# Performance work log

Measured on AMD Instinct MI355X. Metric: run time of the kernel, lower is better.

The kernel has to match this reference:

```python
import jax, jax.numpy as jnp
import numpy as np

# (in_dim, out_dim) for fc1..fc14, hard-coded in the torch module
DIMS = [(12,12),(12,11),(11,10),(10,9),(9,8),(8,7),(7,6),(6,7),(7,8),(8,9),(9,10),(10,11),(11,12),(12,2)]
BATCH = 2_000_000


def setup_inputs() -> dict:
    key = jax.random.key(0)
    keys = jax.random.split(key, 2 * len(DIMS) + 1)
    inp = {"x": jax.random.normal(keys[0], (BATCH, 12), dtype=jnp.float32)}
    for i, (din, dout) in enumerate(DIMS):
        s = 1.0 / np.sqrt(din)  # torch nn.Linear default init range
        inp[f"w{i+1}"] = jax.random.uniform(keys[2*i+1], (dout, din), jnp.float32, -s, s)
        inp[f"b{i+1}"] = jax.random.uniform(keys[2*i+2], (dout,), jnp.float32, -s, s)
    return inp


def _forward(x, Ws, Bs):
    lin = lambda h, i: h @ Ws[i].T + Bs[i]
    # encoder half: fc1..fc6 with ReLU, saving identities 1..6
    ids = []
    h = x
    for i in range(6):
        h = jax.nn.relu(lin(h, i))
        ids.append(h)
    # bottleneck fc7
    h = jax.nn.relu(lin(h, 6))
    # decoder half: fc8..fc13, each adds the matching identity before ReLU
    # fc8 (+id6), fc9 (+id5), ..., fc13 (+id1)
    for i in range(7, 13):
        h = jax.nn.relu(lin(h, i) + ids[12 - i])
    # fc14 + softmax over class dim
    return jax.nn.softmax(lin(h, 13), axis=1)


def reference(x, w1, b1, w2, b2, w3, b3, w4, b4, w5, b5, w6, b6, w7, b7,
              w8, b8, w9, b9, w10, b10, w11, b11, w12, b12, w13, b13, w14, b14):
    Ws = [w1, w2, w3, w4, w5, w6, w7, w8, w9, w10, w11, w12, w13, w14]
    Bs = [b1, b2, b3, b4, b5, b6, b7, b8, b9, b10, b11, b12, b13, b14]
    return _forward(x, Ws, Bs)
```

## Files before the change

kernel.cpp:

```cpp
#include <hip/hip_runtime.h>
#include <math.h>

#define DEV __device__ __forceinline__

typedef float f2 __attribute__((ext_vector_type(2)));

DEV f2 splat(float s) { f2 r; r.x = s; r.y = s; return r; }


#define OW1  0
#define OB1  144
#define OW2  156
#define OB2  288
#define OW3  300
#define OB3  412
#define OW4  424
#define OB4  516
#define OW5  528
#define OB5  600
#define OW6  608
#define OB6  664
#define OW7  672
#define OB7  716
#define OW8  724
#define OB8  768
#define OW9  776
#define OB9  832
#define OW10 840
#define OB10 912
#define OW11 924
#define OB11 1016
#define OW12 1028
#define OB12 1140
#define OW13 1152
#define OB13 1284
#define OW14 1296
#define OB14 1320
#define WTOT 1324

__device__ __attribute__((aligned(16))) float Wpack[WTOT];

__global__ void repack_kernel(
    const float* w1,  const float* b1,  const float* w2,  const float* b2,
    const float* w3,  const float* b3,  const float* w4,  const float* b4,
    const float* w5,  const float* b5,  const float* w6,  const float* b6,
    const float* w7,  const float* b7,  const float* w8,  const float* b8,
    const float* w9,  const float* b9,  const float* w10, const float* b10,
    const float* w11, const float* b11, const float* w12, const float* b12,
    const float* w13, const float* b13, const float* w14, const float* b14) {
    struct Seg { const float* src; int dst; int len; };
    const Seg segs[28] = {
        {w1,  OW1,  144}, {b1,  OB1,  12}, {w2,  OW2,  132}, {b2,  OB2,  11},
        {w3,  OW3,  110}, {b3,  OB3,  10}, {w4,  OW4,   90}, {b4,  OB4,   9},
        {w5,  OW5,   72}, {b5,  OB5,   8}, {w6,  OW6,   56}, {b6,  OB6,   7},
        {w7,  OW7,   42}, {b7,  OB7,   6}, {w8,  OW8,   42}, {b8,  OB8,   7},
        {w9,  OW9,   56}, {b9,  OB9,   8}, {w10, OW10,  72}, {b10, OB10,  9},
        {w11, OW11,  90}, {b11, OB11, 10}, {w12, OW12, 110}, {b12, OB12, 11},
        {w13, OW13, 132}, {b13, OB13, 12}, {w14, OW14,  24}, {b14, OB14,  2}};
    const int tid = threadIdx.x;
    for (int s = 0; s < 28; ++s)
        for (int i = tid; i < segs[s].len; i += 256)
            Wpack[segs[s].dst + i] = segs[s].src[i];
}

template <int DIN, int DOUT, int WO, int BO>
DEV void lin2(const f2* in, f2* out) {
    const float* __restrict__ w =
        (const float*)__builtin_assume_aligned(&Wpack[WO], 16);
    const float* __restrict__ b = &Wpack[BO];
#pragma unroll
    for (int ot = 0; ot < DOUT; ot += 4) {
        const int oe = (ot + 4 < DOUT) ? (ot + 4) : DOUT;
        float wt[48];
#pragma unroll
        for (int i = 0; i < 48; ++i) {
            if (i < (oe - ot) * DIN) wt[i] = w[ot * DIN + i];
        }
#pragma unroll
        for (int o = ot; o < oe; ++o) out[o] = splat(b[o]);
#pragma unroll
        for (int k = 0; k < DIN; ++k) {
            f2 xk = in[k];
#pragma unroll
            for (int o = ot; o < oe; ++o)
                out[o] = __builtin_elementwise_fma(
                    xk, splat(wt[(o - ot) * DIN + k]), out[o]);
        }
    }
}

template <int DIN, int DOUT, int WO, int BO>
DEV void lin2_skip(const f2* in, const f2* skip, f2* out) {
    const float* __restrict__ w =
        (const float*)__builtin_assume_aligned(&Wpack[WO], 16);
    const float* __restrict__ b = &Wpack[BO];
#pragma unroll
    for (int ot = 0; ot < DOUT; ot += 4) {
        const int oe = (ot + 4 < DOUT) ? (ot + 4) : DOUT;
        float wt[48];
#pragma unroll
        for (int i = 0; i < 48; ++i) {
            if (i < (oe - ot) * DIN) wt[i] = w[ot * DIN + i];
        }
#pragma unroll
        for (int o = ot; o < oe; ++o) out[o] = splat(b[o]) + skip[o];
#pragma unroll
        for (int k = 0; k < DIN; ++k) {
            f2 xk = in[k];
#pragma unroll
            for (int o = ot; o < oe; ++o)
                out[o] = __builtin_elementwise_fma(
                    xk, splat(wt[(o - ot) * DIN + k]), out[o]);
        }
    }
}

template <int N>
DEV void relu_ip(f2* v) {
#pragma unroll
    for (int k = 0; k < N; ++k) v[k] = __builtin_elementwise_max(v[k], splat(0.0f));
}

__global__ void __launch_bounds__(256, 2)
csnet14_kernel(const float* __restrict__ x, float* __restrict__ out, int nt) {
    int t = blockIdx.x * blockDim.x + threadIdx.x;
    if (t >= nt) return;

    const float4* xr = reinterpret_cast<const float4*>(x + (size_t)t * 24);
    float4 a0 = xr[0], a1 = xr[1], a2 = xr[2];
    float4 a3 = xr[3], a4 = xr[4], a5 = xr[5];
    float r0[12] = {a0.x, a0.y, a0.z, a0.w, a1.x, a1.y, a1.z, a1.w,
                    a2.x, a2.y, a2.z, a2.w};
    float r1[12] = {a3.x, a3.y, a3.z, a3.w, a4.x, a4.y, a4.z, a4.w,
                    a5.x, a5.y, a5.z, a5.w};
    f2 h0[12];
#pragma unroll
    for (int k = 0; k < 12; ++k) { h0[k].x = r0[k]; h0[k].y = r1[k]; }

    f2 id1[12]; lin2<12, 12, OW1, OB1>(h0,  id1); relu_ip<12>(id1);
    f2 id2[11]; lin2<12, 11, OW2, OB2>(id1, id2); relu_ip<11>(id2);
    f2 id3[10]; lin2<11, 10, OW3, OB3>(id2, id3); relu_ip<10>(id3);
    f2 id4[9];  lin2<10,  9, OW4, OB4>(id3, id4); relu_ip<9>(id4);
    f2 id5[8];  lin2< 9,  8, OW5, OB5>(id4, id5); relu_ip<8>(id5);
    f2 id6[7];  lin2< 8,  7, OW6, OB6>(id5, id6); relu_ip<7>(id6);

    f2 t7[6];   lin2< 7,  6, OW7, OB7>(id6, t7);  relu_ip<6>(t7);

    f2 t8[7];   lin2_skip< 6,  7, OW8,  OB8 >(t7,  id6, t8);  relu_ip<7>(t8);
    f2 t9[8];   lin2_skip< 7,  8, OW9,  OB9 >(t8,  id5, t9);  relu_ip<8>(t9);
    f2 t10[9];  lin2_skip< 8,  9, OW10, OB10>(t9,  id4, t10); relu_ip<9>(t10);
    f2 t11[10]; lin2_skip< 9, 10, OW11, OB11>(t10, id3, t11); relu_ip<10>(t11);
    f2 t12[11]; lin2_skip<10, 11, OW12, OB12>(t11, id2, t12); relu_ip<11>(t12);
    f2 t13[12]; lin2_skip<11, 12, OW13, OB13>(t12, id1, t13); relu_ip<12>(t13);

    f2 l[2];    lin2<12,  2, OW14, OB14>(t13, l);
    f2 m  = __builtin_elementwise_max(l[0], l[1]);
    f2 d0 = l[0] - m;
    f2 d1 = l[1] - m;
    float e0a = __expf(d0.x), e0b = __expf(d0.y);
    float e1a = __expf(d1.x), e1b = __expf(d1.y);
    float inva = __builtin_amdgcn_rcpf(e0a + e1a);
    float invb = __builtin_amdgcn_rcpf(e0b + e1b);

    float4 o;
    o.x = e0a * inva;
    o.y = e1a * inva;
    o.z = e0b * invb;
    o.w = e1b * invb;
    reinterpret_cast<float4*>(out)[t] = o;
}

extern "C" void kernel_launch(void* const* d_in, const int* in_sizes, int n_in,
                              void* d_out, int out_size, void* d_ws, size_t ws_size,
                              hipStream_t stream) {
    const float* x   = (const float*)d_in[0];
    const float* w1  = (const float*)d_in[1];  const float* b1  = (const float*)d_in[2];
    const float* w2  = (const float*)d_in[3];  const float* b2  = (const float*)d_in[4];
    const float* w3  = (const float*)d_in[5];  const float* b3  = (const float*)d_in[6];
    const float* w4  = (const float*)d_in[7];  const float* b4  = (const float*)d_in[8];
    const float* w5  = (const float*)d_in[9];  const float* b5  = (const float*)d_in[10];
    const float* w6  = (const float*)d_in[11]; const float* b6  = (const float*)d_in[12];
    const float* w7  = (const float*)d_in[13]; const float* b7  = (const float*)d_in[14];
    const float* w8  = (const float*)d_in[15]; const float* b8  = (const float*)d_in[16];
    const float* w9  = (const float*)d_in[17]; const float* b9  = (const float*)d_in[18];
    const float* w10 = (const float*)d_in[19]; const float* b10 = (const float*)d_in[20];
    const float* w11 = (const float*)d_in[21]; const float* b11 = (const float*)d_in[22];
    const float* w12 = (const float*)d_in[23]; const float* b12 = (const float*)d_in[24];
    const float* w13 = (const float*)d_in[25]; const float* b13 = (const float*)d_in[26];
    const float* w14 = (const float*)d_in[27]; const float* b14 = (const float*)d_in[28];
    float* out = (float*)d_out;

    const int n  = in_sizes[0] / 12;
    const int nt = n / 2;

    repack_kernel<<<1, 256, 0, stream>>>(
        w1, b1, w2, b2, w3, b3, w4, b4, w5, b5, w6, b6, w7, b7,
        w8, b8, w9, b9, w10, b10, w11, b11, w12, b12, w13, b13, w14, b14);

    dim3 block(256);
    dim3 grid((nt + 255) / 256);
    csnet14_kernel<<<grid, block, 0, stream>>>(x, out, nt);
}
```

Baseline: 237.9 us.

## Store skip activations as packed fp16 and raise occupancy to 4 blocks

The encoder identity tensors kept live for the decoder skip connections are now stored as packed half-precision pairs. This halves the registers they occupy across the network, and the launch bound now asks for 4 blocks per SM instead of 2. The goal is higher occupancy to hide latency in this register-heavy per-thread MLP. The cost is extra convert instructions and a loss of precision in the skip additions.

```diff
diff --git a/kernel.cpp b/kernel.cpp
--- a/kernel.cpp
+++ b/kernel.cpp
@@ -4,8 +4,12 @@
 #define DEV __device__ __forceinline__
 
 typedef float f2 __attribute__((ext_vector_type(2)));
+typedef _Float16 h2 __attribute__((ext_vector_type(2)));
 
 DEV f2 splat(float s) { f2 r; r.x = s; r.y = s; return r; }
+
+DEV h2 pk(f2 v) { h2 r; r.x = (_Float16)v.x; r.y = (_Float16)v.y; return r; }
+DEV f2 unpk(h2 h) { f2 r; r.x = (float)h.x; r.y = (float)h.y; return r; }
 
 
 #define OW1  0
@@ -90,7 +94,7 @@
 }
 
 template <int DIN, int DOUT, int WO, int BO>
-DEV void lin2_skip(const f2* in, const f2* skip, f2* out) {
+DEV void lin2_skip(const f2* in, const h2* skip, f2* out) {
     const float* __restrict__ w =
         (const float*)__builtin_assume_aligned(&Wpack[WO], 16);
     const float* __restrict__ b = &Wpack[BO];
@@ -103,7 +107,7 @@
             if (i < (oe - ot) * DIN) wt[i] = w[ot * DIN + i];
         }
 #pragma unroll
-        for (int o = ot; o < oe; ++o) out[o] = splat(b[o]) + skip[o];
+        for (int o = ot; o < oe; ++o) out[o] = splat(b[o]) + unpk(skip[o]);
 #pragma unroll
         for (int k = 0; k < DIN; ++k) {
             f2 xk = in[k];
@@ -121,7 +125,13 @@
     for (int k = 0; k < N; ++k) v[k] = __builtin_elementwise_max(v[k], splat(0.0f));
 }
 
-__global__ void __launch_bounds__(256, 2)
+template <int N>
+DEV void pack_id(const f2* v, h2* p) {
+#pragma unroll
+    for (int k = 0; k < N; ++k) p[k] = pk(v[k]);
+}
+
+__global__ void __launch_bounds__(256, 4)
 csnet14_kernel(const float* __restrict__ x, float* __restrict__ out, int nt) {
     int t = blockIdx.x * blockDim.x + threadIdx.x;
     if (t >= nt) return;
@@ -138,20 +148,26 @@
     for (int k = 0; k < 12; ++k) { h0[k].x = r0[k]; h0[k].y = r1[k]; }
 
     f2 id1[12]; lin2<12, 12, OW1, OB1>(h0,  id1); relu_ip<12>(id1);
+    h2 p1[12];  pack_id<12>(id1, p1);
     f2 id2[11]; lin2<12, 11, OW2, OB2>(id1, id2); relu_ip<11>(id2);
+    h2 p2[11];  pack_id<11>(id2, p2);
     f2 id3[10]; lin2<11, 10, OW3, OB3>(id2, id3); relu_ip<10>(id3);
+    h2 p3[10];  pack_id<10>(id3, p3);
     f2 id4[9];  lin2<10,  9, OW4, OB4>(id3, id4); relu_ip<9>(id4);
+    h2 p4[9];   pack_id<9>(id4, p4);
     f2 id5[8];  lin2< 9,  8, OW5, OB5>(id4, id5); relu_ip<8>(id5);
+    h2 p5[8];   pack_id<8>(id5, p5);
     f2 id6[7];  lin2< 8,  7, OW6, OB6>(id5, id6); relu_ip<7>(id6);
+    h2 p6[7];   pack_id<7>(id6, p6);
 
     f2 t7[6];   lin2< 7,  6, OW7, OB7>(id6, t7);  relu_ip<6>(t7);
 
-    f2 t8[7];   lin2_skip< 6,  7, OW8,  OB8 >(t7,  id6, t8);  relu_ip<7>(t8);
-    f2 t9[8];   lin2_skip< 7,  8, OW9,  OB9 >(t8,  id5, t9);  relu_ip<8>(t9);
-    f2 t10[9];  lin2_skip< 8,  9, OW10, OB10>(t9,  id4, t10); relu_ip<9>(t10);
-    f2 t11[10]; lin2_skip< 9, 10, OW11, OB11>(t10, id3, t11); relu_ip<10>(t11);
-    f2 t12[11]; lin2_skip<10, 11, OW12, OB12>(t11, id2, t12); relu_ip<11>(t12);
-    f2 t13[12]; lin2_skip<11, 12, OW13, OB13>(t12, id1, t13); relu_ip<12>(t13);
+    f2 t8[7];   lin2_skip< 6,  7, OW8,  OB8 >(t7,  p6, t8);  relu_ip<7>(t8);
+    f2 t9[8];   lin2_skip< 7,  8, OW9,  OB9 >(t8,  p5, t9);  relu_ip<8>(t9);
+    f2 t10[9];  lin2_skip< 8,  9, OW10, OB10>(t9,  p4, t10); relu_ip<9>(t10);
+    f2 t11[10]; lin2_skip< 9, 10, OW11, OB11>(t10, p3, t11); relu_ip<10>(t11);
+    f2 t12[11]; lin2_skip<10, 11, OW12, OB12>(t11, p2, t12); relu_ip<11>(t12);
+    f2 t13[12]; lin2_skip<11, 12, OW13, OB13>(t12, p1, t13); relu_ip<12>(t13);
 
     f2 l[2];    lin2<12,  2, OW14, OB14>(t13, l);
     f2 m  = __builtin_elementwise_max(l[0], l[1]);
```

Result: no change. 237.7 us (-0.1%).
